# Kernel optimization log

Hardware: AMD Instinct MI355X
Metric: run time of the kernel (lower is better)

Reference implementation:

```python
import jax, jax.numpy as jnp
import numpy as np

EMBED_DIM = 1024
NUM_HEADS = 16
HEAD_DIM = EMBED_DIM // NUM_HEADS
ROPE_BASE = 10000.0


def setup_inputs() -> dict:
    key = jax.random.key(0)
    ks = jax.random.split(key, 5)
    B, S, E = 4, 2048, EMBED_DIM
    hidden = jax.random.normal(ks[0], (B, S, E), dtype=jnp.float32)
    sc_in = 1.0 / np.sqrt(E)
    qkv_w = jax.random.normal(ks[1], (3 * E, E), dtype=jnp.float32) * sc_in
    qkv_b = jnp.zeros((3 * E,), dtype=jnp.float32)
    proj_w = jax.random.normal(ks[2], (E, E), dtype=jnp.float32) * sc_in
    proj_b = jnp.zeros((E,), dtype=jnp.float32)
    return {"hidden": hidden, "qkv_w": qkv_w, "qkv_b": qkv_b,
            "proj_w": proj_w, "proj_b": proj_b}


def _rope_cos_sin(position_ids, head_dim, base):
    # position_ids: [B, S] int; returns cos/sin of shape [B, 1, S, head_dim]
    inv_freq = 1.0 / (base ** (jnp.arange(0, head_dim, 2, dtype=jnp.float32) / head_dim))
    freqs = position_ids.astype(jnp.float32)[..., None] * inv_freq  # [B,S,hd/2]
    emb = jnp.concatenate([freqs, freqs], axis=-1)                  # [B,S,hd]
    return jnp.cos(emb)[:, None], jnp.sin(emb)[:, None]


def _rotate_half(x):
    x1, x2 = jnp.split(x, 2, axis=-1)
    return jnp.concatenate([-x2, x1], axis=-1)


def reference(hidden, qkv_w, qkv_b, proj_w, proj_b):
    B, S, E = hidden.shape
    H, hd = NUM_HEADS, HEAD_DIM
    qkv = hidden @ qkv_w.T + qkv_b                    # [B,S,3E]
    qkv = qkv.reshape(B, S, 3, H, hd).transpose(2, 0, 3, 1, 4)  # [3,B,H,S,hd]
    q, k, v = qkv[0], qkv[1], qkv[2]
    pos = jnp.broadcast_to(jnp.arange(S)[None, :], (B, S))
    cos, sin = _rope_cos_sin(pos, hd, ROPE_BASE)      # [B,1,S,hd]
    q = q * cos + _rotate_half(q) * sin
    k = k * cos + _rotate_half(k) * sin
    scale = 1.0 / jnp.sqrt(jnp.float32(hd))
    scores = jnp.einsum("bhsd,bhtd->bhst", q, k) * scale
    attn = jax.nn.softmax(scores, axis=-1)
    out = jnp.einsum("bhst,bhtd->bhsd", attn, v)      # [B,H,S,hd]
    out = out.transpose(0, 2, 1, 3).reshape(B, S, E)
    return out @ proj_w.T + proj_b
```

## Files before the change

### kernel.cpp

```cpp
#include <hip/hip_runtime.h>
#include <cstdint>
#include <cstddef>

typedef _Float16 f16;
typedef __attribute__((ext_vector_type(4))) float f32x4;
typedef __attribute__((ext_vector_type(8))) _Float16 f16x8;
typedef __attribute__((ext_vector_type(4))) _Float16 f16x4;

#define S_SEQ 2048
#define E_DIM 1024

#define OFF_HID   0ull
#define OFF_QKVW  8388608ull
#define OFF_PROJW 11534336ull
#define OFF_Q     12582912ull
#define OFF_K     20971520ull
#define OFF_VT    29360128ull
#define OFF_AO    37748736ull

__device__ __forceinline__ void async_copy16(const void* g, void* l) {
  __builtin_amdgcn_global_load_lds(
      (const __attribute__((address_space(1))) unsigned int*)g,
      (__attribute__((address_space(3))) unsigned int*)l, 16, 0, 0);
}

__device__ __forceinline__ float fast_exp2(float x) {
#if __has_builtin(__builtin_amdgcn_exp2f)
  return __builtin_amdgcn_exp2f(x);
#else
  return __expf(x * 0.6931471805599453f);
#endif
}

__global__ __launch_bounds__(256) void cvt_kernel(const float* __restrict__ hid,
                                                  const float* __restrict__ qw,
                                                  const float* __restrict__ pw,
                                                  f16* __restrict__ ws) {
  long i = (long)blockIdx.x * 256 + threadIdx.x;
  const float* src;
  f16* dst;
  long idx;
  if (i < 2097152L) { src = hid; dst = ws + OFF_HID;  idx = i; }
  else if (i < 2883584L) { src = qw; dst = ws + OFF_QKVW; idx = i - 2097152L; }
  else { src = pw; dst = ws + OFF_PROJW; idx = i - 2883584L; }
  float4 v = *(const float4*)(src + idx * 4);
  f16x4 o = { (f16)v.x, (f16)v.y, (f16)v.z, (f16)v.w };
  *(f16x4*)(dst + idx * 4) = o;
}

template <int MODE>
__global__ __launch_bounds__(256)
void gemm_kernel(const f16* __restrict__ A, const f16* __restrict__ Bm,
                 const float* __restrict__ bias,
                 f16* __restrict__ q_out, f16* __restrict__ k_out,
                 f16* __restrict__ vT_out, float* __restrict__ f_out) {
  __shared__ __align__(16) f16 As[2][128 * 32];
  __shared__ __align__(16) f16 Bs[2][128 * 32];
  const int tid = threadIdx.x;
  const int wave = tid >> 6;
  const int lane = tid & 63;
  const int q4 = lane >> 4;
  const int l16 = lane & 15;
  const int m0 = blockIdx.y * 128;
  const int n0 = blockIdx.x * 128;
  const int wr = (wave >> 1) * 64;
  const int wc = (wave & 1) * 64;
  f32x4 acc[4][4] = {};

  const int srow = tid >> 2;
  const int scol = (tid & 3) * 8;

  auto stage = [&](int k0, int b) {
    for (int p = 0; p < 2; ++p) {
      int row = p * 64 + srow;
      async_copy16(A + (size_t)(m0 + row) * 1024 + k0 + scol,
                   &As[b][(size_t)(p * 256 + wave * 64) * 8]);
      async_copy16(Bm + (size_t)(n0 + row) * 1024 + k0 + scol,
                   &Bs[b][(size_t)(p * 256 + wave * 64) * 8]);
    }
  };

  stage(0, 0);
  __syncthreads();
  int buf = 0;
  for (int k0 = 0; k0 < 1024; k0 += 32) {
    if (k0 + 32 < 1024) stage(k0 + 32, buf ^ 1);
    f16x8 af[4], bf[4];
    for (int mt = 0; mt < 4; ++mt)
      af[mt] = *(const f16x8*)&As[buf][(wr + mt * 16 + l16) * 32 + q4 * 8];
    for (int nt = 0; nt < 4; ++nt)
      bf[nt] = *(const f16x8*)&Bs[buf][(wc + nt * 16 + l16) * 32 + q4 * 8];
    for (int mt = 0; mt < 4; ++mt)
      for (int nt = 0; nt < 4; ++nt)
        acc[mt][nt] = __builtin_amdgcn_mfma_f32_16x16x32_f16(af[mt], bf[nt],
                                                             acc[mt][nt], 0, 0, 0);
    __syncthreads();
    buf ^= 1;
  }

  if constexpr (MODE == 0) {
    const int bx = blockIdx.x;
    const int part = bx >> 3;
    const int h = (((bx & 7) * 128) + wc) >> 6;
    float bv[4];
    for (int nt = 0; nt < 4; ++nt) bv[nt] = bias[n0 + wc + nt * 16 + l16];
    if (part < 2) {
      f16* outp = (part == 0) ? q_out : k_out;
      const float qscale = (part == 0) ? 0.18033688011112042f : 1.0f;
      float invf[2];
      for (int nt = 0; nt < 2; ++nt)
        invf[nt] = __expf(-(float)(nt * 16 + l16) * 0.2878231366242557f);
      for (int mt = 0; mt < 4; ++mt) {
        int mbase = m0 + wr + mt * 16 + q4 * 4;
        for (int r = 0; r < 4; ++r) {
          int mm = mbase + r;
          int b = mm >> 11, s = mm & 2047;
          size_t rowb = ((size_t)((b * 16 + h) * 2048 + s)) * 64;
          for (int nt = 0; nt < 2; ++nt) {
            float x1 = acc[mt][nt][r] + bv[nt];
            float x2 = acc[mt][nt + 2][r] + bv[nt + 2];
            float ang = (float)s * invf[nt];
            float sn, cs;
            __sincosf(ang, &sn, &cs);
            float o1 = (x1 * cs - x2 * sn) * qscale;
            float o2 = (x2 * cs + x1 * sn) * qscale;
            int d1 = nt * 16 + l16;
            outp[rowb + d1] = (f16)o1;
            outp[rowb + d1 + 32] = (f16)o2;
          }
        }
      }
    } else {
      for (int mt = 0; mt < 4; ++mt) {
        int mbase = m0 + wr + mt * 16 + q4 * 4;
        int b = mbase >> 11, s0 = mbase & 2047;
        for (int nt = 0; nt < 4; ++nt) {
          int d = nt * 16 + l16;
          size_t basei = ((size_t)((b * 16 + h) * 64 + d)) * 2048 + s0;
          f16x4 pk;
          for (int r = 0; r < 4; ++r) pk[r] = (f16)(acc[mt][nt][r] + bv[nt]);
          *(f16x4*)&vT_out[basei] = pk;
        }
      }
    }
  } else {
    float bv[4];
    for (int nt = 0; nt < 4; ++nt) bv[nt] = bias[n0 + wc + nt * 16 + l16];
    for (int mt = 0; mt < 4; ++mt)
      for (int r = 0; r < 4; ++r) {
        int mm = m0 + wr + mt * 16 + q4 * 4 + r;
        for (int nt = 0; nt < 4; ++nt)
          f_out[(size_t)mm * 1024 + n0 + wc + nt * 16 + l16] = acc[mt][nt][r] + bv[nt];
      }
  }
}

__global__ __launch_bounds__(256, 4)
void attn_kernel(const f16* __restrict__ Qg, const f16* __restrict__ Kg,
                 const f16* __restrict__ VTg, f16* __restrict__ AOg) {
  __shared__ __align__(16) f16 smem[2][2 * 64 * 72];
  const int tid = threadIdx.x;
  const int wave = tid >> 6, lane = tid & 63;
  const int q4 = lane >> 4, l16 = lane & 15;
  const int qt = blockIdx.x, bh = blockIdx.y;
  const f16* Qb = Qg + (size_t)bh * (S_SEQ * 64);
  const f16* Kb = Kg + (size_t)bh * (S_SEQ * 64);
  const f16* Vb = VTg + (size_t)bh * (64 * S_SEQ);
  const int ws0 = wave * 32;

  f16x8 qf[2][2];
  for (int sn = 0; sn < 2; ++sn)
    for (int kf = 0; kf < 2; ++kf)
      qf[sn][kf] = *(const f16x8*)(Qb + (size_t)(qt * 128 + ws0 + sn * 16 + l16) * 64
                                      + kf * 32 + q4 * 8);

  f32x4 o[4][2] = {};
  float lsum[2] = {0.f, 0.f};

  const int srow = tid >> 3;
  const int scol = (tid & 7) * 8;

  int4 k0r = *(const int4*)(Kb + (size_t)srow * 64 + scol);
  int4 k1r = *(const int4*)(Kb + (size_t)(32 + srow) * 64 + scol);
  int4 v0r = *(const int4*)(Vb + (size_t)srow * 2048 + scol);
  int4 v1r = *(const int4*)(Vb + (size_t)(32 + srow) * 2048 + scol);
  {
    f16* Kn = smem[0];
    f16* Vn = smem[0] + 64 * 72;
    *(int4*)(Kn + srow * 72 + scol) = k0r;
    *(int4*)(Kn + (32 + srow) * 72 + scol) = k1r;
    *(int4*)(Vn + srow * 72 + scol) = v0r;
    *(int4*)(Vn + (32 + srow) * 72 + scol) = v1r;
  }
  __syncthreads();

  int cur = 0;
  for (int tt = 0; tt < 32; ++tt) {
    const f16* Kc = smem[cur];
    const f16* Vc = smem[cur] + 64 * 72;

    if (tt + 1 < 32) {
      const int t0n = (tt + 1) * 64;
      k0r = *(const int4*)(Kb + (size_t)(t0n + srow) * 64 + scol);
      k1r = *(const int4*)(Kb + (size_t)(t0n + 32 + srow) * 64 + scol);
      v0r = *(const int4*)(Vb + (size_t)srow * 2048 + t0n + scol);
      v1r = *(const int4*)(Vb + (size_t)(32 + srow) * 2048 + t0n + scol);
    }

    f32x4 st[4][2];
    for (int tm = 0; tm < 4; ++tm) {
      f16x8 k0 = *(const f16x8*)(Kc + (tm * 16 + l16) * 72 + q4 * 8);
      f16x8 k1 = *(const f16x8*)(Kc + (tm * 16 + l16) * 72 + 32 + q4 * 8);
      for (int sn = 0; sn < 2; ++sn) {
        f32x4 c = {0.f, 0.f, 0.f, 0.f};
        c = __builtin_amdgcn_mfma_f32_16x16x32_f16(k0, qf[sn][0], c, 0, 0, 0);
        c = __builtin_amdgcn_mfma_f32_16x16x32_f16(k1, qf[sn][1], c, 0, 0, 0);
        st[tm][sn] = c;
      }
    }

    for (int sn = 0; sn < 2; ++sn) {
      float rs = 0.f;
      for (int tm = 0; tm < 4; ++tm)
        for (int r = 0; r < 4; ++r) {
          float p = fast_exp2(st[tm][sn][r]);
          st[tm][sn][r] = p;
          rs += p;
        }
      lsum[sn] += rs;
    }

    for (int tm = 0; tm < 4; ++tm) {
      f16x4 vfr[4];
      for (int dm = 0; dm < 4; ++dm)
        vfr[dm] = *(const f16x4*)(Vc + (dm * 16 + l16) * 72 + tm * 16 + q4 * 4);
      for (int sn = 0; sn < 2; ++sn) {
        f16x4 pfr;
        pfr[0] = (f16)st[tm][sn][0];
        pfr[1] = (f16)st[tm][sn][1];
        pfr[2] = (f16)st[tm][sn][2];
        pfr[3] = (f16)st[tm][sn][3];
        for (int dm = 0; dm < 4; ++dm)
          o[dm][sn] = __builtin_amdgcn_mfma_f32_16x16x16f16(vfr[dm], pfr,
                                                            o[dm][sn], 0, 0, 0);
      }
    }

    if (tt + 1 < 32) {
      f16* Kn = smem[cur ^ 1];
      f16* Vn = smem[cur ^ 1] + 64 * 72;
      *(int4*)(Kn + srow * 72 + scol) = k0r;
      *(int4*)(Kn + (32 + srow) * 72 + scol) = k1r;
      *(int4*)(Vn + srow * 72 + scol) = v0r;
      *(int4*)(Vn + (32 + srow) * 72 + scol) = v1r;
    }
    __syncthreads();
    cur ^= 1;
  }

  float inv_l[2];
  for (int sn = 0; sn < 2; ++sn) {
    float l = lsum[sn];
    l += __shfl_xor(l, 16, 64);
    l += __shfl_xor(l, 32, 64);
    inv_l[sn] = 1.0f / l;
  }
  f16* Ot = smem[0];
  for (int sn = 0; sn < 2; ++sn) {
    int so = ws0 + sn * 16 + l16;
    for (int dm = 0; dm < 4; ++dm) {
      f16x4 w;
      w[0] = (f16)(o[dm][sn][0] * inv_l[sn]);
      w[1] = (f16)(o[dm][sn][1] * inv_l[sn]);
      w[2] = (f16)(o[dm][sn][2] * inv_l[sn]);
      w[3] = (f16)(o[dm][sn][3] * inv_l[sn]);
      *(f16x4*)(Ot + so * 72 + dm * 16 + q4 * 4) = w;
    }
  }
  __syncthreads();
  const int b = bh >> 4, h = bh & 15;
  const int sr = tid >> 1, dh = (tid & 1) * 32;
  size_t gbase = ((size_t)(b * 2048 + qt * 128 + sr)) * 1024 + h * 64 + dh;
  for (int c = 0; c < 4; ++c) {
    f16x8 v = *(const f16x8*)(Ot + sr * 72 + dh + c * 8);
    *(f16x8*)(AOg + gbase + c * 8) = v;
  }
}

extern "C" void kernel_launch(void* const* d_in, const int* in_sizes, int n_in,
                              void* d_out, int out_size, void* d_ws, size_t ws_size,
                              hipStream_t stream) {
  const float* hid   = (const float*)d_in[0];
  const float* qkvw  = (const float*)d_in[1];
  const float* qkvb  = (const float*)d_in[2];
  const float* projw = (const float*)d_in[3];
  const float* projb = (const float*)d_in[4];
  float* out = (float*)d_out;
  f16* ws = (f16*)d_ws;

  cvt_kernel<<<12288, 256, 0, stream>>>(hid, qkvw, projw, ws);
  gemm_kernel<0><<<dim3(24, 64), 256, 0, stream>>>(
      ws + OFF_HID, ws + OFF_QKVW, qkvb,
      ws + OFF_Q, ws + OFF_K, ws + OFF_VT, nullptr);
  attn_kernel<<<dim3(16, 64), 256, 0, stream>>>(
      ws + OFF_Q, ws + OFF_K, ws + OFF_VT, ws + OFF_AO);
  gemm_kernel<1><<<dim3(8, 64), 256, 0, stream>>>(
      ws + OFF_AO, ws + OFF_PROJW, projb,
      nullptr, nullptr, nullptr, out);
}
```

Baseline: 276.3 us.

## Swizzle GEMM LDS tiles, narrow output-projection tile, remap attention block order

```diff
diff --git a/kernel.cpp b/kernel.cpp
--- a/kernel.cpp
+++ b/kernel.cpp
@@ -48,35 +48,45 @@
   *(f16x4*)(dst + idx * 4) = o;
 }
 
-template <int MODE>
+template <int MODE, int BN>
 __global__ __launch_bounds__(256)
 void gemm_kernel(const f16* __restrict__ A, const f16* __restrict__ Bm,
                  const float* __restrict__ bias,
                  f16* __restrict__ q_out, f16* __restrict__ k_out,
                  f16* __restrict__ vT_out, float* __restrict__ f_out) {
+  constexpr int NT = BN / 32;
   __shared__ __align__(16) f16 As[2][128 * 32];
-  __shared__ __align__(16) f16 Bs[2][128 * 32];
+  __shared__ __align__(16) f16 Bs[2][BN * 32];
   const int tid = threadIdx.x;
   const int wave = tid >> 6;
   const int lane = tid & 63;
   const int q4 = lane >> 4;
   const int l16 = lane & 15;
   const int m0 = blockIdx.y * 128;
-  const int n0 = blockIdx.x * 128;
+  const int n0 = blockIdx.x * BN;
   const int wr = (wave >> 1) * 64;
-  const int wc = (wave & 1) * 64;
-  f32x4 acc[4][4] = {};
+  const int wc = (wave & 1) * (BN / 2);
+  f32x4 acc[4][NT] = {};
 
   const int srow = tid >> 2;
-  const int scol = (tid & 3) * 8;
+  const int scol = (((tid & 3) ^ ((srow >> 1) & 3)) * 8);
+  const int swz = (l16 >> 1) & 3;
 
   auto stage = [&](int k0, int b) {
     for (int p = 0; p < 2; ++p) {
       int row = p * 64 + srow;
       async_copy16(A + (size_t)(m0 + row) * 1024 + k0 + scol,
                    &As[b][(size_t)(p * 256 + wave * 64) * 8]);
-      async_copy16(Bm + (size_t)(n0 + row) * 1024 + k0 + scol,
-                   &Bs[b][(size_t)(p * 256 + wave * 64) * 8]);
+    }
+    if constexpr (BN == 128) {
+      for (int p = 0; p < 2; ++p) {
+        int row = p * 64 + srow;
+        async_copy16(Bm + (size_t)(n0 + row) * 1024 + k0 + scol,
+                     &Bs[b][(size_t)(p * 256 + wave * 64) * 8]);
+      }
+    } else {
+      async_copy16(Bm + (size_t)(n0 + srow) * 1024 + k0 + scol,
+                   &Bs[b][(size_t)(wave * 64) * 8]);
     }
   };
 
@@ -85,13 +95,13 @@
   int buf = 0;
   for (int k0 = 0; k0 < 1024; k0 += 32) {
     if (k0 + 32 < 1024) stage(k0 + 32, buf ^ 1);
-    f16x8 af[4], bf[4];
+    f16x8 af[4], bf[NT];
     for (int mt = 0; mt < 4; ++mt)
-      af[mt] = *(const f16x8*)&As[buf][(wr + mt * 16 + l16) * 32 + q4 * 8];
-    for (int nt = 0; nt < 4; ++nt)
-      bf[nt] = *(const f16x8*)&Bs[buf][(wc + nt * 16 + l16) * 32 + q4 * 8];
+      af[mt] = *(const f16x8*)&As[buf][(wr + mt * 16 + l16) * 32 + (q4 ^ swz) * 8];
+    for (int nt = 0; nt < NT; ++nt)
+      bf[nt] = *(const f16x8*)&Bs[buf][(wc + nt * 16 + l16) * 32 + (q4 ^ swz) * 8];
     for (int mt = 0; mt < 4; ++mt)
-      for (int nt = 0; nt < 4; ++nt)
+      for (int nt = 0; nt < NT; ++nt)
         acc[mt][nt] = __builtin_amdgcn_mfma_f32_16x16x32_f16(af[mt], bf[nt],
                                                              acc[mt][nt], 0, 0, 0);
     __syncthreads();
@@ -144,12 +154,12 @@
       }
     }
   } else {
-    float bv[4];
-    for (int nt = 0; nt < 4; ++nt) bv[nt] = bias[n0 + wc + nt * 16 + l16];
+    float bv[NT];
+    for (int nt = 0; nt < NT; ++nt) bv[nt] = bias[n0 + wc + nt * 16 + l16];
     for (int mt = 0; mt < 4; ++mt)
       for (int r = 0; r < 4; ++r) {
         int mm = m0 + wr + mt * 16 + q4 * 4 + r;
-        for (int nt = 0; nt < 4; ++nt)
+        for (int nt = 0; nt < NT; ++nt)
           f_out[(size_t)mm * 1024 + n0 + wc + nt * 16 + l16] = acc[mt][nt][r] + bv[nt];
       }
   }
@@ -162,7 +172,9 @@
   const int tid = threadIdx.x;
   const int wave = tid >> 6, lane = tid & 63;
   const int q4 = lane >> 4, l16 = lane & 15;
-  const int qt = blockIdx.x, bh = blockIdx.y;
+  const int id = blockIdx.x;
+  const int qt = (id >> 3) & 15;
+  const int bh = (id & 7) * 8 + (id >> 7);
   const f16* Qb = Qg + (size_t)bh * (S_SEQ * 64);
   const f16* Kb = Kg + (size_t)bh * (S_SEQ * 64);
   const f16* Vb = VTg + (size_t)bh * (64 * S_SEQ);
@@ -299,12 +311,12 @@
   f16* ws = (f16*)d_ws;
 
   cvt_kernel<<<12288, 256, 0, stream>>>(hid, qkvw, projw, ws);
-  gemm_kernel<0><<<dim3(24, 64), 256, 0, stream>>>(
+  gemm_kernel<0, 128><<<dim3(24, 64), 256, 0, stream>>>(
       ws + OFF_HID, ws + OFF_QKVW, qkvb,
       ws + OFF_Q, ws + OFF_K, ws + OFF_VT, nullptr);
-  attn_kernel<<<dim3(16, 64), 256, 0, stream>>>(
+  attn_kernel<<<1024, 256, 0, stream>>>(
       ws + OFF_Q, ws + OFF_K, ws + OFF_VT, ws + OFF_AO);
-  gemm_kernel<1><<<dim3(8, 64), 256, 0, stream>>>(
+  gemm_kernel<1, 64><<<dim3(16, 64), 256, 0, stream>>>(
       ws + OFF_AO, ws + OFF_PROJW, projb,
       nullptr, nullptr, nullptr, out);
 }
```

Result: slower. 283.7 us (+2.7%).
